# Performance work log

Hardware: AMD Instinct MI355X
Metric: run time of the kernel (lower is better)

The kernel has to match this reference:

```python
import jax, jax.numpy as jnp
import numpy as np

B, S, NN = 16, 512, 8          # batch, spatial nodes, neighbors per node
IN, H, NHEAD = 128, 512, 4     # input_size, hidden_size, n_head


def _forward(inputs, h, c, h_spatial, a_src, w_fg, b_fg, w_ig, b_ig,
             w_ih, w_hh, b_ih, b_hh):
    N = B * S
    x = inputs.reshape(N, IN)
    h = h.reshape(N, H)
    c = c.reshape(N, H)
    hs = h_spatial.reshape(N, NN, H)

    # attention logits: concat(h, neighbor) @ a_src, split to avoid materializing concat
    a_self, a_nb = a_src[:H], a_src[H:]              # [H, NHEAD] each
    attn = h @ a_self                                  # [N, NHEAD]
    attn = attn[:, None, :] + jnp.einsum('nkh,hm->nkm', hs, a_nb)  # [N, NN, NHEAD]
    attn = jnp.where(attn >= 0, attn, 0.2 * attn)      # leaky_relu(0.2)
    attn = jax.nn.softmax(attn, axis=1)                # softmax over neighbors

    # aggregate neighbors per head -> [N, NHEAD*H]
    agg = jnp.einsum('nkm,nkh->nmh', attn, hs).reshape(N, NHEAD * H)

    spatial_f = jax.nn.sigmoid(agg @ w_fg.T + b_fg)    # [N, H]
    spatial_i = jax.nn.sigmoid(agg @ w_ig.T + b_ig)
    h = h * spatial_i
    c = c * spatial_f

    # torch LSTMCell: gate order i, f, g, o
    gates = x @ w_ih.T + b_ih + h @ w_hh.T + b_hh      # [N, 4H]
    i_g, f_g, g_g, o_g = jnp.split(gates, 4, axis=1)
    i_g = jax.nn.sigmoid(i_g)
    f_g = jax.nn.sigmoid(f_g)
    g_g = jnp.tanh(g_g)
    o_g = jax.nn.sigmoid(o_g)
    c_new = f_g * c + i_g * g_g
    h_new = o_g * jnp.tanh(c_new)
    return h_new.reshape(B, S, H), c_new.reshape(B, S, H)


def setup_inputs() -> dict:
    key = jax.random.key(0)
    ks = jax.random.split(key, 16)
    xav = lambda k, shp: jax.random.uniform(
        k, shp, jnp.float32, -1.0, 1.0) * np.sqrt(6.0 / (shp[0] + shp[1]))
    return {
        'inputs': jax.random.normal(ks[0], (B, S, IN), jnp.float32),
        'h': jax.random.normal(ks[1], (B, S, H), jnp.float32),
        'c': jax.random.normal(ks[2], (B, S, H), jnp.float32),
        'h_spatial': jax.random.normal(ks[3], (B, S, NN, H), jnp.float32),
        'a_src': xav(ks[4], (2 * H, NHEAD)),
        'w_fg': jax.random.normal(ks[5], (H, NHEAD * H), jnp.float32) * 0.02,
        'b_fg': jnp.zeros((H,), jnp.float32),
        'w_ig': jax.random.normal(ks[6], (H, NHEAD * H), jnp.float32) * 0.02,
        'b_ig': jnp.zeros((H,), jnp.float32),
        'w_ih': jax.random.normal(ks[7], (4 * H, IN), jnp.float32) * 0.02,
        'w_hh': jax.random.normal(ks[8], (4 * H, H), jnp.float32) * 0.02,
        'b_ih': jnp.zeros((4 * H,), jnp.float32),
        'b_hh': jnp.zeros((4 * H,), jnp.float32),
    }


def reference(inputs, h, c, h_spatial, a_src, w_fg, b_fg, w_ig, b_ig,
              w_ih, w_hh, b_ih, b_hh):
    return _forward(inputs, h, c, h_spatial, a_src, w_fg, b_fg, w_ig, b_ig,
                    w_ih, w_hh, b_ih, b_hh)
```

## Files before the change

### kernel.cpp

```cpp
#include <hip/hip_runtime.h>
#include <hip/hip_bf16.h>
#include <cstdint>
#include <cstddef>

#define N_ROWS 8192
#define HDIM 512
#define INDIM 128
#define NHEADS 4
#define NNB 8

typedef __bf16 bf16_t;
typedef __bf16 bf16x8 __attribute__((ext_vector_type(8)));
typedef __bf16 bf16x4 __attribute__((ext_vector_type(4)));
typedef __bf16 bf16x2 __attribute__((ext_vector_type(2)));
typedef float f32x4 __attribute__((ext_vector_type(4)));

__device__ __forceinline__ float sigmoidf_(float x) { return 1.0f / (1.0f + expf(-x)); }

__device__ __forceinline__ void load_lds16(const void* g, void* l) {
  __builtin_amdgcn_global_load_lds(
      (const __attribute__((address_space(1))) void*)g,
      (__attribute__((address_space(3))) void*)l, 16, 0, 0);
}

__global__ __launch_bounds__(256) void pack_kernel(
    const float* __restrict__ w_fg, const float* __restrict__ w_ig,
    const float* __restrict__ w_ih, const float* __restrict__ w_hh,
    const float* __restrict__ b_ih, const float* __restrict__ b_hh,
    const float* __restrict__ x,
    bf16_t* __restrict__ W1, bf16_t* __restrict__ W2i,
    float* __restrict__ b2, bf16_t* __restrict__ A2)
{
  int idx = blockIdx.x * 256 + threadIdx.x;
  if (idx < 524288) {
    const int e = idx * 4, r = e >> 11, k = e & 2047;
    const float* src = (r < 512) ? &w_fg[(size_t)r * 2048 + k]
                                 : &w_ig[(size_t)(r - 512) * 2048 + k];
    const float4 v = *(const float4*)src;
    bf16x4 o; o[0] = (bf16_t)v.x; o[1] = (bf16_t)v.y; o[2] = (bf16_t)v.z; o[3] = (bf16_t)v.w;
    *(bf16x4*)&W1[e] = o;
    return;
  }
  idx -= 524288;
  if (idx < 327680) {
    const int e = idx * 4, r = e / 640, k = e - r * 640;
    const int rp = (r & 511) * 4 + (r >> 9);
    const float* src = (k < 128) ? &w_ih[(size_t)r * 128 + k]
                                 : &w_hh[(size_t)r * 512 + (k - 128)];
    const float4 v = *(const float4*)src;
    bf16x4 o; o[0] = (bf16_t)v.x; o[1] = (bf16_t)v.y; o[2] = (bf16_t)v.z; o[3] = (bf16_t)v.w;
    *(bf16x4*)&W2i[(size_t)rp * 640 + k] = o;
    return;
  }
  idx -= 327680;
  if (idx < 2048) {
    const int q = idx >> 2, g = idx & 3;
    b2[idx] = b_ih[g * 512 + q] + b_hh[g * 512 + q];
    return;
  }
  idx -= 2048;
  if (idx < 262144) {
    const int e = idx * 4, n = e >> 7, cc = e & 127;
    const float4 v = *(const float4*)&x[e];
    bf16x4 o; o[0] = (bf16_t)v.x; o[1] = (bf16_t)v.y; o[2] = (bf16_t)v.z; o[3] = (bf16_t)v.w;
    *(bf16x4*)&A2[(size_t)n * 640 + cc] = o;
  }
}

__global__ __launch_bounds__(256) void attn_agg_kernel(
    const float* __restrict__ h, const float* __restrict__ hs,
    const float* __restrict__ a_src, bf16_t* __restrict__ agg)
{
  __shared__ float s_hs[NNB][HDIM];
  __shared__ float s_h[HDIM];
  __shared__ float s_logit[NNB][NHEADS];
  __shared__ float s_self[NHEADS];

  const int n = blockIdx.x;
  const int t = threadIdx.x;
  const float* hs_n = hs + (size_t)n * (NNB * HDIM);
  const float* h_n  = h  + (size_t)n * HDIM;

  {
    const float4* s4 = (const float4*)hs_n;
    float4* d4 = (float4*)&s_hs[0][0];
#pragma unroll
    for (int i = 0; i < 4; ++i) d4[t + i * 256] = s4[t + i * 256];
    if (t < HDIM / 4) ((float4*)s_h)[t] = ((const float4*)h_n)[t];
  }
  __syncthreads();

  const int wave = t >> 6, lane = t & 63;
#pragma unroll
  for (int kk = 0; kk < 2; ++kk) {
    const int k = wave * 2 + kk;
    float acc0 = 0.f, acc1 = 0.f, acc2 = 0.f, acc3 = 0.f;
#pragma unroll
    for (int i = 0; i < HDIM / 64; ++i) {
      const int hh = i * 64 + lane;
      const float v = s_hs[k][hh];
      const float4 av = *(const float4*)(a_src + (size_t)(HDIM + hh) * NHEADS);
      acc0 += v * av.x; acc1 += v * av.y; acc2 += v * av.z; acc3 += v * av.w;
    }
    float accs[NHEADS] = {acc0, acc1, acc2, acc3};
#pragma unroll
    for (int m = 0; m < NHEADS; ++m) {
      float a = accs[m];
#pragma unroll
      for (int off = 32; off > 0; off >>= 1) a += __shfl_xor(a, off);
      if (lane == 0) s_logit[k][m] = a;
    }
  }
  if (wave == 0) {
    float acc0 = 0.f, acc1 = 0.f, acc2 = 0.f, acc3 = 0.f;
#pragma unroll
    for (int i = 0; i < HDIM / 64; ++i) {
      const int hh = i * 64 + lane;
      const float v = s_h[hh];
      const float4 av = *(const float4*)(a_src + (size_t)hh * NHEADS);
      acc0 += v * av.x; acc1 += v * av.y; acc2 += v * av.z; acc3 += v * av.w;
    }
    float accs[NHEADS] = {acc0, acc1, acc2, acc3};
#pragma unroll
    for (int m = 0; m < NHEADS; ++m) {
      float a = accs[m];
#pragma unroll
      for (int off = 32; off > 0; off >>= 1) a += __shfl_xor(a, off);
      if (lane == 0) s_self[m] = a;
    }
  }
  __syncthreads();

  float w[NNB][NHEADS];
#pragma unroll
  for (int m = 0; m < NHEADS; ++m) {
    const float sm = s_self[m];
    float mx = -1e30f;
#pragma unroll
    for (int k = 0; k < NNB; ++k) {
      float l = sm + s_logit[k][m];
      l = (l >= 0.f) ? l : 0.2f * l;
      w[k][m] = l;
      mx = fmaxf(mx, l);
    }
    float sum = 0.f;
#pragma unroll
    for (int k = 0; k < NNB; ++k) { const float e = expf(w[k][m] - mx); w[k][m] = e; sum += e; }
    const float inv = 1.f / sum;
#pragma unroll
    for (int k = 0; k < NNB; ++k) w[k][m] *= inv;
  }

  bf16_t* agg_n = agg + (size_t)n * (NHEADS * HDIM);
  const int hh = t * 2;
  float e0[NNB], e1[NNB];
#pragma unroll
  for (int k = 0; k < NNB; ++k) { e0[k] = s_hs[k][hh]; e1[k] = s_hs[k][hh + 1]; }
#pragma unroll
  for (int m = 0; m < NHEADS; ++m) {
    float a0 = 0.f, a1 = 0.f;
#pragma unroll
    for (int k = 0; k < NNB; ++k) { a0 += w[k][m] * e0[k]; a1 += w[k][m] * e1[k]; }
    bf16x2 pk; pk[0] = (bf16_t)a0; pk[1] = (bf16_t)a1;
    *(bf16x2*)(agg_n + m * HDIM + hh) = pk;
  }
}

__global__ __launch_bounds__(256) void gemm1_kernel(
    const bf16_t* __restrict__ A, const bf16_t* __restrict__ Bt,
    const float* __restrict__ b_fg, const float* __restrict__ b_ig,
    const float* __restrict__ c_in, const float* __restrict__ h_in,
    float* __restrict__ cprime, bf16_t* __restrict__ A2)
{
  __shared__ bf16_t At[128][64];
  __shared__ bf16_t Bs[64][64];

  const int tid  = threadIdx.x;
  const int wave = tid >> 6, lane = tid & 63;
  const int wr = wave >> 1, wc = wave & 1;
  const int bm0 = blockIdx.x * 128;
  const int bn0 = blockIdx.y * 64;
  const int K = 2048;

  f32x4 acc[4][2] = {};

  const int srow = tid >> 3;
  const int sch  = tid & 7;
  const int gsw8 = (sch ^ (srow & 7)) * 8;
  const int sch8 = sch * 8;
  const int frow = lane & 15;
  const int fq   = lane >> 4;

  for (int k0 = 0; k0 < K; k0 += 64) {
#pragma unroll
    for (int r = 0; r < 4; ++r)
      load_lds16(A + (size_t)(bm0 + r * 32 + srow) * K + k0 + gsw8,
                 &At[r * 32 + srow][sch8]);
#pragma unroll
    for (int r = 0; r < 2; ++r)
      load_lds16(Bt + (size_t)(bn0 + r * 32 + srow) * K + k0 + gsw8,
                 &Bs[r * 32 + srow][sch8]);
    __syncthreads();

#pragma unroll
    for (int kk = 0; kk < 2; ++kk) {
      const int fro8 = ((kk * 4 + fq) ^ (frow & 7)) * 8;
      bf16x8 af[4], bv[2];
#pragma unroll
      for (int i = 0; i < 4; ++i)
        af[i] = *(const bf16x8*)&At[wr * 64 + i * 16 + frow][fro8];
#pragma unroll
      for (int j = 0; j < 2; ++j)
        bv[j] = *(const bf16x8*)&Bs[wc * 32 + j * 16 + frow][fro8];
#pragma unroll
      for (int i = 0; i < 4; ++i)
#pragma unroll
        for (int j = 0; j < 2; ++j)
          acc[i][j] = __builtin_amdgcn_mfma_f32_16x16x32_bf16(af[i], bv[j], acc[i][j], 0, 0, 0);
    }
    __syncthreads();
  }

  const int col_in = lane & 15;
  const int row_in = (lane >> 4) * 4;
#pragma unroll
  for (int i = 0; i < 4; ++i) {
#pragma unroll
    for (int j = 0; j < 2; ++j) {
      const int col = bn0 + wc * 32 + j * 16 + col_in;
#pragma unroll
      for (int r = 0; r < 4; ++r) {
        const int row = bm0 + wr * 64 + i * 16 + row_in + r;
        const float v = acc[i][j][r];
        if (col < 512) {
          const float s = sigmoidf_(v + b_fg[col]);
          cprime[(size_t)row * 512 + col] = c_in[(size_t)row * 512 + col] * s;
        } else {
          const int jj = col - 512;
          const float s = sigmoidf_(v + b_ig[jj]);
          A2[(size_t)row * 640 + 128 + jj] = (bf16_t)(h_in[(size_t)row * 512 + jj] * s);
        }
      }
    }
  }
}

__global__ __launch_bounds__(256) void gemm2_kernel(
    const bf16_t* __restrict__ A, const bf16_t* __restrict__ Bt,
    const float* __restrict__ b2, const float* __restrict__ cprime,
    float* __restrict__ out)
{
  __shared__ union {
    struct { bf16_t A[128][64]; bf16_t B[128][64]; } st;
    float epi[64][128];
  } sm;

  const int tid  = threadIdx.x;
  const int wave = tid >> 6, lane = tid & 63;
  const int wr = wave >> 1, wc = wave & 1;
  const int bm0 = blockIdx.x * 128;
  const int bn0 = blockIdx.y * 128;
  const int K = 640;

  f32x4 acc[4][4] = {};

  const int srow = tid >> 3;
  const int sch  = tid & 7;
  const int gsw8 = (sch ^ (srow & 7)) * 8;
  const int sch8 = sch * 8;
  const int frow = lane & 15;
  const int fq   = lane >> 4;

  for (int k0 = 0; k0 < K; k0 += 64) {
#pragma unroll
    for (int r = 0; r < 4; ++r)
      load_lds16(A + (size_t)(bm0 + r * 32 + srow) * K + k0 + gsw8,
                 &sm.st.A[r * 32 + srow][sch8]);
#pragma unroll
    for (int r = 0; r < 4; ++r)
      load_lds16(Bt + (size_t)(bn0 + r * 32 + srow) * K + k0 + gsw8,
                 &sm.st.B[r * 32 + srow][sch8]);
    __syncthreads();

#pragma unroll
    for (int kk = 0; kk < 2; ++kk) {
      const int fro8 = ((kk * 4 + fq) ^ (frow & 7)) * 8;
      bf16x8 af[4], bv[4];
#pragma unroll
      for (int i = 0; i < 4; ++i)
        af[i] = *(const bf16x8*)&sm.st.A[wr * 64 + i * 16 + frow][fro8];
#pragma unroll
      for (int j = 0; j < 4; ++j)
        bv[j] = *(const bf16x8*)&sm.st.B[wc * 64 + j * 16 + frow][fro8];
#pragma unroll
      for (int i = 0; i < 4; ++i)
#pragma unroll
        for (int j = 0; j < 4; ++j)
          acc[i][j] = __builtin_amdgcn_mfma_f32_16x16x32_bf16(af[i], bv[j], acc[i][j], 0, 0, 0);
    }
    __syncthreads();
  }

  const int col_in = lane & 15;
  const int row_in = (lane >> 4) * 4;
  const int q0i = bn0 >> 2;
  const int qi  = tid & 31;
  const int r0  = tid >> 5;

#pragma unroll
  for (int p = 0; p < 2; ++p) {
    if (wr == p) {
#pragma unroll
      for (int i = 0; i < 4; ++i)
#pragma unroll
        for (int j = 0; j < 4; ++j)
#pragma unroll
          for (int r = 0; r < 4; ++r)
            sm.epi[i * 16 + row_in + r][wc * 64 + j * 16 + col_in] = acc[i][j][r];
    }
    __syncthreads();
    const float4 bb = *(const float4*)&b2[(size_t)(q0i + qi) * 4];
#pragma unroll
    for (int rr = 0; rr < 8; ++rr) {
      const int lr = r0 + rr * 8;
      const float4 g4 = *(const float4*)&sm.epi[lr][qi * 4];
      const int grow = bm0 + p * 64 + lr;
      const int q    = q0i + qi;
      const float cp = cprime[(size_t)grow * 512 + q];
      const float ig = sigmoidf_(g4.x + bb.x);
      const float fg = sigmoidf_(g4.y + bb.y);
      const float gg = tanhf(g4.z + bb.z);
      const float og = sigmoidf_(g4.w + bb.w);
      const float cn = fg * cp + ig * gg;
      const float hn = og * tanhf(cn);
      out[(size_t)grow * 512 + q] = hn;
      out[(size_t)N_ROWS * 512 + (size_t)grow * 512 + q] = cn;
    }
    __syncthreads();
  }
}

extern "C" void kernel_launch(void* const* d_in, const int* in_sizes, int n_in,
                              void* d_out, int out_size, void* d_ws, size_t ws_size,
                              hipStream_t stream) {
  const float* x     = (const float*)d_in[0];
  const float* h     = (const float*)d_in[1];
  const float* c     = (const float*)d_in[2];
  const float* hsp   = (const float*)d_in[3];
  const float* a_src = (const float*)d_in[4];
  const float* w_fg  = (const float*)d_in[5];
  const float* b_fg  = (const float*)d_in[6];
  const float* w_ig  = (const float*)d_in[7];
  const float* b_ig  = (const float*)d_in[8];
  const float* w_ih  = (const float*)d_in[9];
  const float* w_hh  = (const float*)d_in[10];
  const float* b_ih  = (const float*)d_in[11];
  const float* b_hh  = (const float*)d_in[12];
  float* out = (float*)d_out;

  uint8_t* ws = (uint8_t*)d_ws;
  bf16_t* agg    = (bf16_t*)(ws);
  bf16_t* W1     = (bf16_t*)(ws + 33554432);
  bf16_t* W2i    = (bf16_t*)(ws + 37748736);
  float*  b2     = (float*) (ws + 40370176);
  bf16_t* A2     = (bf16_t*)(ws + 40378368);
  float*  cprime = (float*) (ws + 50864128);

  pack_kernel<<<4360, 256, 0, stream>>>(w_fg, w_ig, w_ih, w_hh, b_ih, b_hh, x,
                                        W1, W2i, b2, A2);
  attn_agg_kernel<<<N_ROWS, 256, 0, stream>>>(h, hsp, a_src, agg);
  gemm1_kernel<<<dim3(64, 16), 256, 0, stream>>>(
      agg, W1, b_fg, b_ig, c, h, cprime, A2);
  gemm2_kernel<<<dim3(64, 16), 256, 0, stream>>>(
      A2, W2i, b2, cprime, out);
}
```

Measured before the change: 186.2 us.

## Double-buffer LDS K-tiles in both GEMM kernels with 32-wide K steps

Both GEMM kernels switch from single-buffered 64-wide K tiles to two 32-wide K buffers. The next tile's global-to-LDS load is issued before computing the current one, so load latency overlaps MFMA work. The swizzle is reworked for 4 chunks per row. This halves the MFMA work per barrier and doubles the number of syncs. The global_load_lds writes are not explicitly waited on before the barrier, so correctness depends on the compiler inserting vmcnt waits.

```diff
diff --git a/kernel.cpp b/kernel.cpp
--- a/kernel.cpp
+++ b/kernel.cpp
@@ -172,8 +172,8 @@
     const float* __restrict__ c_in, const float* __restrict__ h_in,
     float* __restrict__ cprime, bf16_t* __restrict__ A2)
 {
-  __shared__ bf16_t At[128][64];
-  __shared__ bf16_t Bs[64][64];
+  __shared__ bf16_t At[2][128][32];
+  __shared__ bf16_t Bs[2][64][32];
 
   const int tid  = threadIdx.x;
   const int wave = tid >> 6, lane = tid & 63;
@@ -184,40 +184,37 @@
 
   f32x4 acc[4][2] = {};
 
-  const int srow = tid >> 3;
-  const int sch  = tid & 7;
-  const int gsw8 = (sch ^ (srow & 7)) * 8;
+  const int srow = tid >> 2;
+  const int sch  = tid & 3;
+  const int gsw8 = (sch ^ ((srow >> 1) & 3)) * 8;
   const int sch8 = sch * 8;
   const int frow = lane & 15;
-  const int fq   = lane >> 4;
-
-  for (int k0 = 0; k0 < K; k0 += 64) {
-#pragma unroll
-    for (int r = 0; r < 4; ++r)
-      load_lds16(A + (size_t)(bm0 + r * 32 + srow) * K + k0 + gsw8,
-                 &At[r * 32 + srow][sch8]);
-#pragma unroll
-    for (int r = 0; r < 2; ++r)
-      load_lds16(Bt + (size_t)(bn0 + r * 32 + srow) * K + k0 + gsw8,
-                 &Bs[r * 32 + srow][sch8]);
-    __syncthreads();
-
-#pragma unroll
-    for (int kk = 0; kk < 2; ++kk) {
-      const int fro8 = ((kk * 4 + fq) ^ (frow & 7)) * 8;
-      bf16x8 af[4], bv[2];
-#pragma unroll
-      for (int i = 0; i < 4; ++i)
-        af[i] = *(const bf16x8*)&At[wr * 64 + i * 16 + frow][fro8];
+  const int fro8 = ((lane >> 4) ^ ((frow >> 1) & 3)) * 8;
+
+  auto STAGE = [&](int buf, int k0) {
+    load_lds16(A  + (size_t)(bm0 + srow)      * K + k0 + gsw8, &At[buf][srow][sch8]);
+    load_lds16(A  + (size_t)(bm0 + 64 + srow) * K + k0 + gsw8, &At[buf][64 + srow][sch8]);
+    load_lds16(Bt + (size_t)(bn0 + srow)      * K + k0 + gsw8, &Bs[buf][srow][sch8]);
+  };
+  auto COMPUTE = [&](int buf) {
+    bf16x8 af[4], bv[2];
+#pragma unroll
+    for (int i = 0; i < 4; ++i) af[i] = *(const bf16x8*)&At[buf][wr * 64 + i * 16 + frow][fro8];
+#pragma unroll
+    for (int j = 0; j < 2; ++j) bv[j] = *(const bf16x8*)&Bs[buf][wc * 32 + j * 16 + frow][fro8];
+#pragma unroll
+    for (int i = 0; i < 4; ++i)
 #pragma unroll
       for (int j = 0; j < 2; ++j)
-        bv[j] = *(const bf16x8*)&Bs[wc * 32 + j * 16 + frow][fro8];
-#pragma unroll
-      for (int i = 0; i < 4; ++i)
-#pragma unroll
-        for (int j = 0; j < 2; ++j)
-          acc[i][j] = __builtin_amdgcn_mfma_f32_16x16x32_bf16(af[i], bv[j], acc[i][j], 0, 0, 0);
-    }
+        acc[i][j] = __builtin_amdgcn_mfma_f32_16x16x32_bf16(af[i], bv[j], acc[i][j], 0, 0, 0);
+  };
+
+  const int nt = K >> 5;
+  STAGE(0, 0);
+  __syncthreads();
+  for (int t = 0; t < nt; ++t) {
+    if (t + 1 < nt) STAGE((t + 1) & 1, (t + 1) * 32);
+    COMPUTE(t & 1);
     __syncthreads();
   }
 
@@ -251,7 +248,7 @@
     float* __restrict__ out)
 {
   __shared__ union {
-    struct { bf16_t A[128][64]; bf16_t B[128][64]; } st;
+    struct { bf16_t A[2][128][32]; bf16_t B[2][128][32]; } st;
     float epi[64][128];
   } sm;
 
@@ -264,40 +261,38 @@
 
   f32x4 acc[4][4] = {};
 
-  const int srow = tid >> 3;
-  const int sch  = tid & 7;
-  const int gsw8 = (sch ^ (srow & 7)) * 8;
+  const int srow = tid >> 2;
+  const int sch  = tid & 3;
+  const int gsw8 = (sch ^ ((srow >> 1) & 3)) * 8;
   const int sch8 = sch * 8;
   const int frow = lane & 15;
-  const int fq   = lane >> 4;
-
-  for (int k0 = 0; k0 < K; k0 += 64) {
-#pragma unroll
-    for (int r = 0; r < 4; ++r)
-      load_lds16(A + (size_t)(bm0 + r * 32 + srow) * K + k0 + gsw8,
-                 &sm.st.A[r * 32 + srow][sch8]);
-#pragma unroll
-    for (int r = 0; r < 4; ++r)
-      load_lds16(Bt + (size_t)(bn0 + r * 32 + srow) * K + k0 + gsw8,
-                 &sm.st.B[r * 32 + srow][sch8]);
-    __syncthreads();
-
-#pragma unroll
-    for (int kk = 0; kk < 2; ++kk) {
-      const int fro8 = ((kk * 4 + fq) ^ (frow & 7)) * 8;
-      bf16x8 af[4], bv[4];
-#pragma unroll
-      for (int i = 0; i < 4; ++i)
-        af[i] = *(const bf16x8*)&sm.st.A[wr * 64 + i * 16 + frow][fro8];
+  const int fro8 = ((lane >> 4) ^ ((frow >> 1) & 3)) * 8;
+
+  auto STAGE = [&](int buf, int k0) {
+    load_lds16(A  + (size_t)(bm0 + srow)      * K + k0 + gsw8, &sm.st.A[buf][srow][sch8]);
+    load_lds16(A  + (size_t)(bm0 + 64 + srow) * K + k0 + gsw8, &sm.st.A[buf][64 + srow][sch8]);
+    load_lds16(Bt + (size_t)(bn0 + srow)      * K + k0 + gsw8, &sm.st.B[buf][srow][sch8]);
+    load_lds16(Bt + (size_t)(bn0 + 64 + srow) * K + k0 + gsw8, &sm.st.B[buf][64 + srow][sch8]);
+  };
+  auto COMPUTE = [&](int buf) {
+    bf16x8 af[4], bv[4];
+#pragma unroll
+    for (int i = 0; i < 4; ++i) af[i] = *(const bf16x8*)&sm.st.A[buf][wr * 64 + i * 16 + frow][fro8];
+#pragma unroll
+    for (int j = 0; j < 4; ++j) bv[j] = *(const bf16x8*)&sm.st.B[buf][wc * 64 + j * 16 + frow][fro8];
+#pragma unroll
+    for (int i = 0; i < 4; ++i)
 #pragma unroll
       for (int j = 0; j < 4; ++j)
-        bv[j] = *(const bf16x8*)&sm.st.B[wc * 64 + j * 16 + frow][fro8];
-#pragma unroll
-      for (int i = 0; i < 4; ++i)
-#pragma unroll
-        for (int j = 0; j < 4; ++j)
-          acc[i][j] = __builtin_amdgcn_mfma_f32_16x16x32_bf16(af[i], bv[j], acc[i][j], 0, 0, 0);
-    }
+        acc[i][j] = __builtin_amdgcn_mfma_f32_16x16x32_bf16(af[i], bv[j], acc[i][j], 0, 0, 0);
+  };
+
+  const int nt = K >> 5;
+  STAGE(0, 0);
+  __syncthreads();
+  for (int t = 0; t < nt; ++t) {
+    if (t + 1 < nt) STAGE((t + 1) & 1, (t + 1) * 32);
+    COMPUTE(t & 1);
     __syncthreads();
   }
 
```

New measurement: 188.8 us. No clear change (+1.4%).

## Use two-wave blocks with larger per-wave tiles and BK=32 in both GEMMs

Applied to the files above, without the earlier changes.

Both GEMM kernels go from 4 waves to 2 waves per block, and each wave now covers a larger output tile (64x64 in gemm1, 64x128 in gemm2), so each LDS fragment is reused across more MFMAs. The K step drops from 64 to 32, which changes the LDS swizzle to a 4-chunk pattern and halves LDS use per stage. The epilogue scratch gains padding (132 columns) to reduce bank conflicts. In exchange there are twice as many barrier-separated K iterations, fewer waves to hide latency, and higher accumulator register pressure, which may lower occupancy.

```diff
diff --git a/kernel.cpp b/kernel.cpp
--- a/kernel.cpp
+++ b/kernel.cpp
@@ -166,32 +166,31 @@
   }
 }
 
-__global__ __launch_bounds__(256) void gemm1_kernel(
+__global__ __launch_bounds__(128) void gemm1_kernel(
     const bf16_t* __restrict__ A, const bf16_t* __restrict__ Bt,
     const float* __restrict__ b_fg, const float* __restrict__ b_ig,
     const float* __restrict__ c_in, const float* __restrict__ h_in,
     float* __restrict__ cprime, bf16_t* __restrict__ A2)
 {
-  __shared__ bf16_t At[128][64];
-  __shared__ bf16_t Bs[64][64];
+  __shared__ bf16_t At[128][32];
+  __shared__ bf16_t Bs[64][32];
 
   const int tid  = threadIdx.x;
   const int wave = tid >> 6, lane = tid & 63;
-  const int wr = wave >> 1, wc = wave & 1;
   const int bm0 = blockIdx.x * 128;
   const int bn0 = blockIdx.y * 64;
   const int K = 2048;
 
-  f32x4 acc[4][2] = {};
-
-  const int srow = tid >> 3;
-  const int sch  = tid & 7;
-  const int gsw8 = (sch ^ (srow & 7)) * 8;
+  f32x4 acc[4][4] = {};
+
+  const int srow = tid >> 2;
+  const int sch  = tid & 3;
+  const int gsw8 = (sch ^ ((srow >> 1) & 3)) * 8;
   const int sch8 = sch * 8;
   const int frow = lane & 15;
-  const int fq   = lane >> 4;
-
-  for (int k0 = 0; k0 < K; k0 += 64) {
+  const int fro8 = ((lane >> 4) ^ ((frow >> 1) & 3)) * 8;
+
+  for (int k0 = 0; k0 < K; k0 += 32) {
 #pragma unroll
     for (int r = 0; r < 4; ++r)
       load_lds16(A + (size_t)(bm0 + r * 32 + srow) * K + k0 + gsw8,
@@ -202,22 +201,18 @@
                  &Bs[r * 32 + srow][sch8]);
     __syncthreads();
 
-#pragma unroll
-    for (int kk = 0; kk < 2; ++kk) {
-      const int fro8 = ((kk * 4 + fq) ^ (frow & 7)) * 8;
-      bf16x8 af[4], bv[2];
-#pragma unroll
-      for (int i = 0; i < 4; ++i)
-        af[i] = *(const bf16x8*)&At[wr * 64 + i * 16 + frow][fro8];
-#pragma unroll
-      for (int j = 0; j < 2; ++j)
-        bv[j] = *(const bf16x8*)&Bs[wc * 32 + j * 16 + frow][fro8];
-#pragma unroll
-      for (int i = 0; i < 4; ++i)
-#pragma unroll
-        for (int j = 0; j < 2; ++j)
-          acc[i][j] = __builtin_amdgcn_mfma_f32_16x16x32_bf16(af[i], bv[j], acc[i][j], 0, 0, 0);
-    }
+    bf16x8 af[4], bv[4];
+#pragma unroll
+    for (int i = 0; i < 4; ++i)
+      af[i] = *(const bf16x8*)&At[wave * 64 + i * 16 + frow][fro8];
+#pragma unroll
+    for (int j = 0; j < 4; ++j)
+      bv[j] = *(const bf16x8*)&Bs[j * 16 + frow][fro8];
+#pragma unroll
+    for (int i = 0; i < 4; ++i)
+#pragma unroll
+      for (int j = 0; j < 4; ++j)
+        acc[i][j] = __builtin_amdgcn_mfma_f32_16x16x32_bf16(af[i], bv[j], acc[i][j], 0, 0, 0);
     __syncthreads();
   }
 
@@ -226,11 +221,11 @@
 #pragma unroll
   for (int i = 0; i < 4; ++i) {
 #pragma unroll
-    for (int j = 0; j < 2; ++j) {
-      const int col = bn0 + wc * 32 + j * 16 + col_in;
+    for (int j = 0; j < 4; ++j) {
+      const int col = bn0 + j * 16 + col_in;
 #pragma unroll
       for (int r = 0; r < 4; ++r) {
-        const int row = bm0 + wr * 64 + i * 16 + row_in + r;
+        const int row = bm0 + wave * 64 + i * 16 + row_in + r;
         const float v = acc[i][j][r];
         if (col < 512) {
           const float s = sigmoidf_(v + b_fg[col]);
@@ -245,33 +240,32 @@
   }
 }
 
-__global__ __launch_bounds__(256) void gemm2_kernel(
+__global__ __launch_bounds__(128) void gemm2_kernel(
     const bf16_t* __restrict__ A, const bf16_t* __restrict__ Bt,
     const float* __restrict__ b2, const float* __restrict__ cprime,
     float* __restrict__ out)
 {
   __shared__ union {
-    struct { bf16_t A[128][64]; bf16_t B[128][64]; } st;
-    float epi[64][128];
+    struct { bf16_t A[128][32]; bf16_t B[128][32]; } st;
+    float epi[64][132];
   } sm;
 
   const int tid  = threadIdx.x;
   const int wave = tid >> 6, lane = tid & 63;
-  const int wr = wave >> 1, wc = wave & 1;
   const int bm0 = blockIdx.x * 128;
   const int bn0 = blockIdx.y * 128;
   const int K = 640;
 
-  f32x4 acc[4][4] = {};
-
-  const int srow = tid >> 3;
-  const int sch  = tid & 7;
-  const int gsw8 = (sch ^ (srow & 7)) * 8;
+  f32x4 acc[4][8] = {};
+
+  const int srow = tid >> 2;
+  const int sch  = tid & 3;
+  const int gsw8 = (sch ^ ((srow >> 1) & 3)) * 8;
   const int sch8 = sch * 8;
   const int frow = lane & 15;
-  const int fq   = lane >> 4;
-
-  for (int k0 = 0; k0 < K; k0 += 64) {
+  const int fro8 = ((lane >> 4) ^ ((frow >> 1) & 3)) * 8;
+
+  for (int k0 = 0; k0 < K; k0 += 32) {
 #pragma unroll
     for (int r = 0; r < 4; ++r)
       load_lds16(A + (size_t)(bm0 + r * 32 + srow) * K + k0 + gsw8,
@@ -282,22 +276,18 @@
                  &sm.st.B[r * 32 + srow][sch8]);
     __syncthreads();
 
-#pragma unroll
-    for (int kk = 0; kk < 2; ++kk) {
-      const int fro8 = ((kk * 4 + fq) ^ (frow & 7)) * 8;
-      bf16x8 af[4], bv[4];
-#pragma unroll
-      for (int i = 0; i < 4; ++i)
-        af[i] = *(const bf16x8*)&sm.st.A[wr * 64 + i * 16 + frow][fro8];
-#pragma unroll
-      for (int j = 0; j < 4; ++j)
-        bv[j] = *(const bf16x8*)&sm.st.B[wc * 64 + j * 16 + frow][fro8];
-#pragma unroll
-      for (int i = 0; i < 4; ++i)
-#pragma unroll
-        for (int j = 0; j < 4; ++j)
-          acc[i][j] = __builtin_amdgcn_mfma_f32_16x16x32_bf16(af[i], bv[j], acc[i][j], 0, 0, 0);
-    }
+    bf16x8 af[4], bv[8];
+#pragma unroll
+    for (int i = 0; i < 4; ++i)
+      af[i] = *(const bf16x8*)&sm.st.A[wave * 64 + i * 16 + frow][fro8];
+#pragma unroll
+    for (int j = 0; j < 8; ++j)
+      bv[j] = *(const bf16x8*)&sm.st.B[j * 16 + frow][fro8];
+#pragma unroll
+    for (int i = 0; i < 4; ++i)
+#pragma unroll
+      for (int j = 0; j < 8; ++j)
+        acc[i][j] = __builtin_amdgcn_mfma_f32_16x16x32_bf16(af[i], bv[j], acc[i][j], 0, 0, 0);
     __syncthreads();
   }
 
@@ -309,20 +299,20 @@
 
 #pragma unroll
   for (int p = 0; p < 2; ++p) {
-    if (wr == p) {
+    if (wave == p) {
 #pragma unroll
       for (int i = 0; i < 4; ++i)
 #pragma unroll
-        for (int j = 0; j < 4; ++j)
+        for (int j = 0; j < 8; ++j)
 #pragma unroll
           for (int r = 0; r < 4; ++r)
-            sm.epi[i * 16 + row_in + r][wc * 64 + j * 16 + col_in] = acc[i][j][r];
+            sm.epi[i * 16 + row_in + r][j * 16 + col_in] = acc[i][j][r];
     }
     __syncthreads();
     const float4 bb = *(const float4*)&b2[(size_t)(q0i + qi) * 4];
 #pragma unroll
-    for (int rr = 0; rr < 8; ++rr) {
-      const int lr = r0 + rr * 8;
+    for (int rr = 0; rr < 16; ++rr) {
+      const int lr = r0 + rr * 4;
       const float4 g4 = *(const float4*)&sm.epi[lr][qi * 4];
       const int grow = bm0 + p * 64 + lr;
       const int q    = q0i + qi;
@@ -369,8 +359,8 @@
   pack_kernel<<<4360, 256, 0, stream>>>(w_fg, w_ig, w_ih, w_hh, b_ih, b_hh, x,
                                         W1, W2i, b2, A2);
   attn_agg_kernel<<<N_ROWS, 256, 0, stream>>>(h, hsp, a_src, agg);
-  gemm1_kernel<<<dim3(64, 16), 256, 0, stream>>>(
+  gemm1_kernel<<<dim3(64, 16), 128, 0, stream>>>(
       agg, W1, b_fg, b_ig, c, h, cprime, A2);
-  gemm2_kernel<<<dim3(64, 16), 256, 0, stream>>>(
+  gemm2_kernel<<<dim3(64, 16), 128, 0, stream>>>(
       A2, W2i, b2, cprime, out);
 }
```

Result: slower. 213.6 us (+14.7%).

## Restructure gemm1 into single-wave blocks with double-buffered async LDS loads

Applied to the files above, without the earlier changes.

Gemm1 now runs one 64-thread wave per block on a 64x64 output tile with a K step of 32, instead of four waves on a 128x64 tile. Two LDS buffers are filled with global_load_lds and tracked by explicit s_waitcnt vmcnt counts, so the load of tile t+2 overlaps compute on tile t and no block barriers remain. The grid doubles to 2048 blocks for more parallelism and latency hiding. In exchange each wave reloads B tiles without sharing them across waves, which raises global and L2 traffic, and the hand-written vmcnt waits depend on the exact number of issued loads.

```diff
diff --git a/kernel.cpp b/kernel.cpp
--- a/kernel.cpp
+++ b/kernel.cpp
@@ -166,71 +166,72 @@
   }
 }
 
-__global__ __launch_bounds__(256) void gemm1_kernel(
+__global__ __launch_bounds__(64) void gemm1_kernel(
     const bf16_t* __restrict__ A, const bf16_t* __restrict__ Bt,
     const float* __restrict__ b_fg, const float* __restrict__ b_ig,
     const float* __restrict__ c_in, const float* __restrict__ h_in,
     float* __restrict__ cprime, bf16_t* __restrict__ A2)
 {
-  __shared__ bf16_t At[128][64];
-  __shared__ bf16_t Bs[64][64];
-
-  const int tid  = threadIdx.x;
-  const int wave = tid >> 6, lane = tid & 63;
-  const int wr = wave >> 1, wc = wave & 1;
-  const int bm0 = blockIdx.x * 128;
+  __shared__ bf16_t At[2][64][32];
+  __shared__ bf16_t Bs[2][64][32];
+
+  const int tid = threadIdx.x;
+  const int bm0 = blockIdx.x * 64;
   const int bn0 = blockIdx.y * 64;
   const int K = 2048;
 
-  f32x4 acc[4][2] = {};
-
-  const int srow = tid >> 3;
-  const int sch  = tid & 7;
-  const int gsw8 = (sch ^ (srow & 7)) * 8;
-  const int sch8 = sch * 8;
-  const int frow = lane & 15;
-  const int fq   = lane >> 4;
-
-  for (int k0 = 0; k0 < K; k0 += 64) {
+  f32x4 acc[4][4] = {};
+
+  const int srow4 = tid >> 2;
+  const int sch   = tid & 3;
+  const int gsw8  = (sch ^ ((srow4 >> 1) & 3)) * 8;
+  const int sch8  = sch * 8;
+  const int frow  = tid & 15;
+  const int fro8  = ((tid >> 4) ^ ((frow >> 1) & 3)) * 8;
+
+  auto STAGE = [&](int buf, int k0) {
 #pragma unroll
     for (int r = 0; r < 4; ++r)
-      load_lds16(A + (size_t)(bm0 + r * 32 + srow) * K + k0 + gsw8,
-                 &At[r * 32 + srow][sch8]);
-#pragma unroll
-    for (int r = 0; r < 2; ++r)
-      load_lds16(Bt + (size_t)(bn0 + r * 32 + srow) * K + k0 + gsw8,
-                 &Bs[r * 32 + srow][sch8]);
-    __syncthreads();
-
-#pragma unroll
-    for (int kk = 0; kk < 2; ++kk) {
-      const int fro8 = ((kk * 4 + fq) ^ (frow & 7)) * 8;
-      bf16x8 af[4], bv[2];
-#pragma unroll
-      for (int i = 0; i < 4; ++i)
-        af[i] = *(const bf16x8*)&At[wr * 64 + i * 16 + frow][fro8];
-#pragma unroll
-      for (int j = 0; j < 2; ++j)
-        bv[j] = *(const bf16x8*)&Bs[wc * 32 + j * 16 + frow][fro8];
-#pragma unroll
-      for (int i = 0; i < 4; ++i)
-#pragma unroll
-        for (int j = 0; j < 2; ++j)
-          acc[i][j] = __builtin_amdgcn_mfma_f32_16x16x32_bf16(af[i], bv[j], acc[i][j], 0, 0, 0);
-    }
-    __syncthreads();
-  }
-
-  const int col_in = lane & 15;
-  const int row_in = (lane >> 4) * 4;
+      load_lds16(A + (size_t)(bm0 + r * 16 + srow4) * K + k0 + gsw8,
+                 &At[buf][r * 16 + srow4][sch8]);
+#pragma unroll
+    for (int r = 0; r < 4; ++r)
+      load_lds16(Bt + (size_t)(bn0 + r * 16 + srow4) * K + k0 + gsw8,
+                 &Bs[buf][r * 16 + srow4][sch8]);
+  };
+  auto COMPUTE = [&](int buf) {
+    bf16x8 af[4], bv[4];
+#pragma unroll
+    for (int i = 0; i < 4; ++i) af[i] = *(const bf16x8*)&At[buf][i * 16 + frow][fro8];
+#pragma unroll
+    for (int j = 0; j < 4; ++j) bv[j] = *(const bf16x8*)&Bs[buf][j * 16 + frow][fro8];
+#pragma unroll
+    for (int i = 0; i < 4; ++i)
+#pragma unroll
+      for (int j = 0; j < 4; ++j)
+        acc[i][j] = __builtin_amdgcn_mfma_f32_16x16x32_bf16(af[i], bv[j], acc[i][j], 0, 0, 0);
+  };
+
+  const int nt = K >> 5;
+  STAGE(0, 0);
+  STAGE(1, 32);
+  for (int t = 0; t < nt; ++t) {
+    if (t < nt - 1) asm volatile("s_waitcnt vmcnt(8)" ::: "memory");
+    else            asm volatile("s_waitcnt vmcnt(0)" ::: "memory");
+    COMPUTE(t & 1);
+    if (t + 2 < nt) STAGE(t & 1, (t + 2) * 32);
+  }
+
+  const int col_in = tid & 15;
+  const int row_in = (tid >> 4) * 4;
 #pragma unroll
   for (int i = 0; i < 4; ++i) {
 #pragma unroll
-    for (int j = 0; j < 2; ++j) {
-      const int col = bn0 + wc * 32 + j * 16 + col_in;
+    for (int j = 0; j < 4; ++j) {
+      const int col = bn0 + j * 16 + col_in;
 #pragma unroll
       for (int r = 0; r < 4; ++r) {
-        const int row = bm0 + wr * 64 + i * 16 + row_in + r;
+        const int row = bm0 + i * 16 + row_in + r;
         const float v = acc[i][j][r];
         if (col < 512) {
           const float s = sigmoidf_(v + b_fg[col]);
@@ -369,7 +370,7 @@
   pack_kernel<<<4360, 256, 0, stream>>>(w_fg, w_ig, w_ih, w_hh, b_ih, b_hh, x,
                                         W1, W2i, b2, A2);
   attn_agg_kernel<<<N_ROWS, 256, 0, stream>>>(h, hsp, a_src, agg);
-  gemm1_kernel<<<dim3(64, 16), 256, 0, stream>>>(
+  gemm1_kernel<<<dim3(128, 16), 64, 0, stream>>>(
       agg, W1, b_fg, b_ig, c, h, cprime, A2);
   gemm2_kernel<<<dim3(64, 16), 256, 0, stream>>>(
       A2, W2i, b2, cprime, out);
```

New measurement: 230.0 us. 1.24x slower.
